# Kernel optimization log

Measured on AMD Instinct MI355X. Metric: run time of the kernel, lower is better.

## Reference

```python
import jax, jax.numpy as jnp
import numpy as np

ORDER = 128


def setup_inputs() -> dict:
    key = jax.random.key(0)
    k1, k2 = jax.random.split(key)
    B, T, p, Tf = 16, 131072, ORDER, 8192
    excitation = jax.random.normal(k1, (B, T), dtype=jnp.float32)
    # reflection coefficients in (-1, 1)
    rc = jax.random.uniform(k2, (B, p, Tf), dtype=jnp.float32, minval=-1.0, maxval=1.0)
    return {"excitation": excitation, "rc": rc}


def _rc_to_lpc(rc):
    """Step-up (Levinson-Durbin) recursion: reflection coeffs -> LPC coeffs.

    rc: (B, p, T_f)  ->  a: (B, T_f, p+1) with a[..., 0] == 1.
    Each step i does a[..., 1:i+2] += k_i * flip(a[..., :i+1]).
    Implemented as a full-width masked gather so it runs in one lax.scan.
    """
    B, p, Tf = rc.shape
    ks = jnp.transpose(rc, (1, 0, 2))  # (p, B, Tf)
    a0 = jnp.zeros((B, Tf, p + 1), rc.dtype).at[..., 0].set(1.0)
    j = jnp.arange(p + 1)

    def step(a, inp):
        i, k = inp  # i: scalar order index, k: (B, Tf)
        src = jnp.clip(i + 1 - j, 0, p)
        a_rev = jnp.take(a, src, axis=-1)          # flipped prefix, full width
        mask = (j >= 1) & (j <= i + 1)             # only positions 1..i+1 update
        a = a + jnp.where(mask, k[..., None] * a_rev, jnp.zeros((), a.dtype))
        return a, None

    a, _ = jax.lax.scan(step, a0, (jnp.arange(p), ks))
    return a


def reference(excitation, rc):
    # forward: rc = rc * 0.98, then step-up recursion to LPC coefficients.
    # (the original module's FFT synthesis path is dead code and the audio
    #  passthrough is the identity; the live math is the recursion below)
    rc = rc * 0.98
    return _rc_to_lpc(rc)
```

## Files before the change

kernel.cpp:

```cpp
#include <hip/hip_runtime.h>


#define NB   16
#define ORD  128
#define TF   8192

template<int M, int J>
struct PairUpd {
    static __device__ __forceinline__ void run(float (&a)[ORD + 1], float k) {
        const float lo = a[J];
        const float hi = a[M - J];
        a[J]     = fmaf(k, hi, lo);
        a[M - J] = fmaf(k, lo, hi);
        if constexpr (2 * (J + 1) < M) PairUpd<M, J + 1>::run(a, k);
    }
};

template<int M>
struct Step {
    static __device__ __forceinline__ void run(float (&a)[ORD + 1],
                                               const float (&kq)[ORD]) {
        const float k = 0.98f * kq[M - 1];
        if constexpr (M > 2) PairUpd<M, 1>::run(a, k);
        if constexpr ((M & 1) == 0) {
            const float mid = a[M / 2];
            a[M / 2] = fmaf(k, mid, mid);
        }
        a[M] = k;
        if constexpr (M < ORD) Step<M + 1>::run(a, kq);
    }
};

template<int J>
struct Stage {
    static __device__ __forceinline__ void run(float* __restrict__ dst,
                                               const float (&a)[ORD + 1]) {
        dst[J] = a[J];
        if constexpr (J < ORD) Stage<J + 1>::run(dst, a);
    }
};

__global__ __launch_bounds__(64)
__attribute__((amdgpu_waves_per_eu(1, 1)))
void lpc_stepup_kernel(const float* __restrict__ rc, float* __restrict__ out) {
    const int lane = threadIdx.x;
    const int gid  = blockIdx.x * 64 + lane;
    const int b = gid >> 13;
    const int t = gid & (TF - 1);
    const float* rcp = rc + ((size_t)b * ORD) * TF + t;

    float kq[ORD];
#pragma unroll
    for (int i = 0; i < ORD; ++i) kq[i] = rcp[(size_t)i * TF];

    float a[ORD + 1];
    a[0] = 1.0f;
    Step<1>::run(a, kq);

    __shared__ __align__(16) float lds[64 * (ORD + 1)];
    Stage<0>::run(&lds[lane * (ORD + 1)], a);
    __syncthreads();

    const float4* lds4 = (const float4*)lds;
    float4* out4 = (float4*)(out + (size_t)blockIdx.x * 64 * (ORD + 1));
#pragma unroll 4
    for (int e = lane; e < (64 * (ORD + 1)) / 4; e += 64)
        out4[e] = lds4[e];
}

extern "C" void kernel_launch(void* const* d_in, const int* in_sizes, int n_in,
                              void* d_out, int out_size, void* d_ws, size_t ws_size,
                              hipStream_t stream) {
    const float* rc = (const float*)d_in[1];
    float* out = (float*)d_out;
    dim3 grid((NB * TF) / 64);
    dim3 block(64);
    hipLaunchKernelGGL(lpc_stepup_kernel, grid, block, 0, stream, rc, out);
}
```

Before: 144.2 us.

## Process two columns per lane with packed float2 FMA and streamed coefficient prefetch

Each lane now handles two time columns, packing them into 2-wide float vectors so the step-up recursion can use packed FMA instructions. The reflection coefficients are no longer all preloaded into registers; an 8-deep ring of vector slots is refilled as each order step is consumed. The output is staged through LDS in two halves with extra barriers. The grid is halved, which reduces the wave count and parallelism in exchange for higher per-instruction throughput, and the 129-element vector accumulator doubles register pressure.

Result: slower. 225.1 us (+56.1%).

```diff
diff --git a/kernel.cpp b/kernel.cpp
--- a/kernel.cpp
+++ b/kernel.cpp
@@ -4,39 +4,55 @@
 #define NB   16
 #define ORD  128
 #define TF   8192
+#define PD   8
+
+typedef __attribute__((ext_vector_type(2))) float v2f;
+
+static __device__ __forceinline__ v2f vfma(v2f a, v2f b, v2f c) {
+    return __builtin_elementwise_fma(a, b, c);
+}
 
 template<int M, int J>
 struct PairUpd {
-    static __device__ __forceinline__ void run(float (&a)[ORD + 1], float k) {
-        const float lo = a[J];
-        const float hi = a[M - J];
-        a[J]     = fmaf(k, hi, lo);
-        a[M - J] = fmaf(k, lo, hi);
-        if constexpr (2 * (J + 1) < M) PairUpd<M, J + 1>::run(a, k);
+    static __device__ __forceinline__ void run(v2f (&A)[ORD + 1], v2f kk) {
+        const v2f lo = A[J];
+        const v2f hi = A[M - J];
+        A[J]     = vfma(kk, hi, lo);
+        A[M - J] = vfma(kk, lo, hi);
+        if constexpr (2 * (J + 1) < M) PairUpd<M, J + 1>::run(A, kk);
     }
 };
 
 template<int M>
 struct Step {
-    static __device__ __forceinline__ void run(float (&a)[ORD + 1],
-                                               const float (&kq)[ORD]) {
-        const float k = 0.98f * kq[M - 1];
-        if constexpr (M > 2) PairUpd<M, 1>::run(a, k);
+    static __device__ __forceinline__ void run(v2f (&A)[ORD + 1],
+                                               v2f (&kq)[PD],
+                                               const float* __restrict__ rcp) {
+        constexpr int slot = (M - 1) & (PD - 1);
+        const v2f kk = kq[slot] * 0.98f;
+        if constexpr (M - 1 + PD < ORD) {
+            v2f nk;
+            nk.x = rcp[(size_t)(M - 1 + PD) * TF];
+            nk.y = rcp[(size_t)(M - 1 + PD) * TF + 64];
+            kq[slot] = nk;
+        }
+        asm volatile("" ::: "memory");
+        if constexpr (M > 2) PairUpd<M, 1>::run(A, kk);
         if constexpr ((M & 1) == 0) {
-            const float mid = a[M / 2];
-            a[M / 2] = fmaf(k, mid, mid);
+            const v2f mid = A[M / 2];
+            A[M / 2] = vfma(kk, mid, mid);
         }
-        a[M] = k;
-        if constexpr (M < ORD) Step<M + 1>::run(a, kq);
+        A[M] = kk;
+        if constexpr (M < ORD) Step<M + 1>::run(A, kq, rcp);
     }
 };
 
-template<int J>
+template<int J, int H>
 struct Stage {
     static __device__ __forceinline__ void run(float* __restrict__ dst,
-                                               const float (&a)[ORD + 1]) {
-        dst[J] = a[J];
-        if constexpr (J < ORD) Stage<J + 1>::run(dst, a);
+                                               const v2f (&A)[ORD + 1]) {
+        dst[J] = (H == 0) ? A[J].x : A[J].y;
+        if constexpr (J < ORD) Stage<J + 1, H>::run(dst, A);
     }
 };
 
@@ -44,28 +60,46 @@
 __attribute__((amdgpu_waves_per_eu(1, 1)))
 void lpc_stepup_kernel(const float* __restrict__ rc, float* __restrict__ out) {
     const int lane = threadIdx.x;
-    const int gid  = blockIdx.x * 64 + lane;
-    const int b = gid >> 13;
-    const int t = gid & (TF - 1);
+    const int col0 = blockIdx.x * 128 + lane;
+    const int b = col0 >> 13;
+    const int t = col0 & (TF - 1);
     const float* rcp = rc + ((size_t)b * ORD) * TF + t;
 
-    float kq[ORD];
+    v2f kq[PD];
 #pragma unroll
-    for (int i = 0; i < ORD; ++i) kq[i] = rcp[(size_t)i * TF];
+    for (int i = 0; i < PD; ++i) {
+        v2f nk;
+        nk.x = rcp[(size_t)i * TF];
+        nk.y = rcp[(size_t)i * TF + 64];
+        kq[i] = nk;
+    }
 
-    float a[ORD + 1];
-    a[0] = 1.0f;
-    Step<1>::run(a, kq);
+    v2f A[ORD + 1];
+    A[0] = (v2f){1.0f, 1.0f};
+    Step<1>::run(A, kq, rcp);
 
     __shared__ __align__(16) float lds[64 * (ORD + 1)];
-    Stage<0>::run(&lds[lane * (ORD + 1)], a);
+    float* out_block = out + (size_t)blockIdx.x * 128 * (ORD + 1);
+
+    Stage<0, 0>::run(&lds[lane * (ORD + 1)], A);
     __syncthreads();
-
-    const float4* lds4 = (const float4*)lds;
-    float4* out4 = (float4*)(out + (size_t)blockIdx.x * 64 * (ORD + 1));
+    {
+        const float4* lds4 = (const float4*)lds;
+        float4* out4 = (float4*)out_block;
 #pragma unroll 4
-    for (int e = lane; e < (64 * (ORD + 1)) / 4; e += 64)
-        out4[e] = lds4[e];
+        for (int e = lane; e < (64 * (ORD + 1)) / 4; e += 64)
+            out4[e] = lds4[e];
+    }
+    __syncthreads();
+    Stage<0, 1>::run(&lds[lane * (ORD + 1)], A);
+    __syncthreads();
+    {
+        const float4* lds4 = (const float4*)lds;
+        float4* out4 = (float4*)(out_block + 64 * (ORD + 1));
+#pragma unroll 4
+        for (int e = lane; e < (64 * (ORD + 1)) / 4; e += 64)
+            out4[e] = lds4[e];
+    }
 }
 
 extern "C" void kernel_launch(void* const* d_in, const int* in_sizes, int n_in,
@@ -73,7 +107,7 @@
                               hipStream_t stream) {
     const float* rc = (const float*)d_in[1];
     float* out = (float*)d_out;
-    dim3 grid((NB * TF) / 64);
+    dim3 grid((NB * TF) / 128);
     dim3 block(64);
     hipLaunchKernelGGL(lpc_stepup_kernel, grid, block, 0, stream, rc, out);
 }
```
